# Optimization experiments

Hardware: AMD Instinct MI355X
Metric: run time of the kernel (lower is better)

## Reference

```python
import jax, jax.numpy as jnp
import numpy as np

B, N, H = 16, 128, 256


def setup_inputs() -> dict:
    key = jax.random.key(0)
    ks = jax.random.split(key, 7)
    s = 1.0 / np.sqrt(H)
    return {
        "inputs": jax.random.normal(ks[0], (B, N, H), dtype=jnp.float32),
        "bin_features": jax.random.normal(ks[1], (B, N, N, H), dtype=jnp.float32),
        "W_atom": jax.random.normal(ks[2], (H, H), dtype=jnp.float32) * s,
        "W_bin": jax.random.normal(ks[3], (H, H), dtype=jnp.float32) * s,
        "b_bin": jax.random.normal(ks[4], (H,), dtype=jnp.float32) * s,
        "w_score": jax.random.normal(ks[5], (H, 1), dtype=jnp.float32) * s,
        "b_score": jax.random.normal(ks[6], (1,), dtype=jnp.float32) * s,
    }


def reference(inputs, bin_features, W_atom, W_bin, b_bin, w_score, b_score):
    # atom_pair[b,i,j,h] = inputs[b,i,h] + inputs[b,j,h]
    atom_pair = inputs[:, :, None, :] + inputs[:, None, :, :]  # [B,N,N,H]
    # Linear(no bias) on atom_pair + Linear(bias) on bin_features, then ReLU.
    # Exploit linearity: (x_i + x_j) @ W = (x@W)_i + (x@W)_j to avoid an extra N^2 GEMM.
    xw = jnp.einsum('bnh,hk->bnk', inputs, W_atom)  # [B,N,H]
    att_hidden = jax.nn.relu(
        xw[:, :, None, :] + xw[:, None, :, :]
        + jnp.einsum('bijh,hk->bijk', bin_features, W_bin) + b_bin
    )  # [B,N,N,H]
    att_score = jnp.einsum('bijh,ho->bijo', att_hidden, w_score) + b_score  # [B,N,N,1]
    # att_context = att_score * inputs.unsqueeze(2); sum over j (dim 2)
    att_context = (att_score * inputs[:, :, None, :]).sum(axis=2)  # [B,N,H]
    return att_context, atom_pair
```

## Files before the change

kernel.cpp:

```cpp
#include <hip/hip_runtime.h>
#include <hip/hip_bf16.h>

#define H 256
#define NN 128
#define BB 16

typedef __attribute__((ext_vector_type(8))) __bf16 bf16x8;
typedef __attribute__((ext_vector_type(8))) short  s16x8;
typedef __attribute__((ext_vector_type(4))) short  s16x4;
typedef __attribute__((ext_vector_type(4))) float  f32x4;

__device__ __forceinline__ unsigned short f2b(float f) {
    unsigned u = __float_as_uint(f);
    u = (u + 0x7fffu + ((u >> 16) & 1u)) >> 16;
    return (unsigned short)u;
}

__global__ void k_prep_w(const float* __restrict__ Wb, unsigned short* __restrict__ WT) {
    int k = blockIdx.x;
    int h = threadIdx.x;
    WT[k * H + h] = f2b(Wb[h * H + k]);
}

__global__ void k_xw(const float* __restrict__ inp, const float* __restrict__ Wa,
                     float* __restrict__ xw) {
    __shared__ float rows[8][H];
    int r0 = blockIdx.x * 8;
    int t = threadIdx.x;
    #pragma unroll
    for (int r = 0; r < 8; ++r) rows[r][t] = inp[(r0 + r) * H + t];
    __syncthreads();
    float acc[8] = {0.f, 0.f, 0.f, 0.f, 0.f, 0.f, 0.f, 0.f};
    for (int h = 0; h < H; ++h) {
        float wv = Wa[h * H + t];
        #pragma unroll
        for (int r = 0; r < 8; ++r) acc[r] += rows[r][h] * wv;
    }
    #pragma unroll
    for (int r = 0; r < 8; ++r) xw[(r0 + r) * H + t] = acc[r];
}

__global__ __launch_bounds__(256) void k_main(
        const float* __restrict__ inp, const float* __restrict__ binf,
        const float* __restrict__ xw, const unsigned short* __restrict__ WT,
        const float* __restrict__ b_bin, const float* __restrict__ w_score,
        const float* __restrict__ b_score,
        float* __restrict__ out_ctx, float* __restrict__ out_pair) {
    __shared__ unsigned short Ab[64 * 260];
    __shared__ float base_l[H];
    __shared__ float wsc_l[H];
    __shared__ float ini_l[H];
    __shared__ float wred[4];
    __shared__ float Sp;

    int bid = blockIdx.x;
    int jt = bid & 1;
    int i  = (bid >> 1) & 127;
    int b  = bid >> 8;
    int t  = threadIdx.x;
    int bi = b * 128 + i;
    int jbase = jt * 64;

    base_l[t] = xw[bi * H + t] + b_bin[t];
    wsc_l[t]  = w_score[t];
    ini_l[t]  = inp[bi * H + t];

    const float4* bp = (const float4*)(binf + ((long)bi * 128 + jbase) * H);
    #pragma unroll
    for (int it = 0; it < 16; ++it) {
        int idx = it * 256 + t;
        float4 v = bp[idx];
        int row = idx >> 6;
        int col = (idx & 63) * 4;
        ushort4 w;
        w.x = f2b(v.x); w.y = f2b(v.y); w.z = f2b(v.z); w.w = f2b(v.w);
        *(ushort4*)&Ab[row * 260 + col] = w;
    }
    __syncthreads();

    int wave = t >> 6, lane = t & 63, q = lane >> 4, m16 = lane & 15;
    int colbase = wave * 64;

    f32x4 acc[4][4];
    #pragma unroll
    for (int rt = 0; rt < 4; ++rt)
        #pragma unroll
        for (int ct = 0; ct < 4; ++ct)
            acc[rt][ct] = (f32x4){0.f, 0.f, 0.f, 0.f};

    #pragma unroll
    for (int ks = 0; ks < 8; ++ks) {
        bf16x8 afr[4];
        #pragma unroll
        for (int rt = 0; rt < 4; ++rt) {
            const unsigned short* p = &Ab[(rt * 16 + m16) * 260 + ks * 32 + q * 8];
            s16x4 a0 = *(const s16x4*)p;
            s16x4 a1 = *(const s16x4*)(p + 4);
            s16x8 sv = __builtin_shufflevector(a0, a1, 0, 1, 2, 3, 4, 5, 6, 7);
            afr[rt] = __builtin_bit_cast(bf16x8, sv);
        }
        #pragma unroll
        for (int ct = 0; ct < 4; ++ct) {
            const unsigned short* wp = WT + (colbase + ct * 16 + m16) * H + ks * 32 + q * 8;
            bf16x8 bfr = __builtin_bit_cast(bf16x8, *(const s16x8*)wp);
            #pragma unroll
            for (int rt = 0; rt < 4; ++rt)
                acc[rt][ct] = __builtin_amdgcn_mfma_f32_16x16x32_bf16(afr[rt], bfr, acc[rt][ct], 0, 0, 0);
        }
    }

    float sacc = 0.f;
    const float* xwp = xw + ((long)b * 128 + jbase) * H;
    #pragma unroll
    for (int rt = 0; rt < 4; ++rt) {
        #pragma unroll
        for (int ct = 0; ct < 4; ++ct) {
            int k = colbase + ct * 16 + m16;
            float bs = base_l[k], wv = wsc_l[k];
            #pragma unroll
            for (int r = 0; r < 4; ++r) {
                int jl = rt * 16 + q * 4 + r;
                float hv = acc[rt][ct][r] + bs + xwp[jl * H + k];
                hv = fmaxf(hv, 0.f);
                sacc += hv * wv;
            }
        }
    }
    #pragma unroll
    for (int m = 1; m < 64; m <<= 1) sacc += __shfl_xor(sacc, m, 64);
    if (lane == 0) wred[wave] = sacc;
    __syncthreads();
    if (t == 0) Sp = wred[0] + wred[1] + wred[2] + wred[3] + 64.0f * b_score[0];
    __syncthreads();

    float iv = ini_l[t];
    float S  = Sp;
    const float* inb  = inp + ((long)b * 128 + jbase) * H;
    float* pout = out_pair + (((long)bi) * 128 + jbase) * H;
    #pragma unroll 4
    for (int j = 0; j < 64; ++j) {
        float v = inb[j * H + t];
        pout[j * H + t] = iv + v;
    }
    atomicAdd(&out_ctx[bi * H + t], iv * S);
}

extern "C" void kernel_launch(void* const* d_in, const int* in_sizes, int n_in,
                              void* d_out, int out_size, void* d_ws, size_t ws_size,
                              hipStream_t stream) {
    const float* inp     = (const float*)d_in[0];
    const float* binf    = (const float*)d_in[1];
    const float* W_atom  = (const float*)d_in[2];
    const float* W_bin   = (const float*)d_in[3];
    const float* b_bin   = (const float*)d_in[4];
    const float* w_score = (const float*)d_in[5];
    const float* b_score = (const float*)d_in[6];

    float* out_ctx  = (float*)d_out;
    float* out_pair = (float*)d_out + BB * NN * H;

    float* xw = (float*)d_ws;
    unsigned short* WT = (unsigned short*)((char*)d_ws + (size_t)BB * NN * H * 4);

    hipMemsetAsync(d_out, 0, (size_t)BB * NN * H * sizeof(float), stream);
    k_prep_w<<<H, H, 0, stream>>>(W_bin, WT);
    k_xw<<<BB * NN / 8, H, 0, stream>>>(inp, W_atom, xw);
    k_main<<<BB * NN * 2, 256, 0, stream>>>(inp, binf, xw, WT, b_bin, w_score,
                                            b_score, out_ctx, out_pair);
}
```

Before: 538.5 us.

## Split pair output into separate kernel and shrink score tiles to 32 rows

Moves the atom_pair broadcast-add into its own float4 streaming kernel and shrinks the score kernel's j-tile from 64 to 32 rows, so it launches four times as many blocks with half the LDS. The weight transpose now goes through a shared-memory tile for coalesced access, and the xw kernel uses 4 rows per block instead of 8. This aims to raise occupancy and separate the pure-bandwidth pair write from the GEMM path. In exchange it adds a launch and doubles the atomicAdd traffic to out_ctx, and the W_bin B-fragments are reused across fewer rows.

```diff
diff --git a/kernel.cpp b/kernel.cpp
--- a/kernel.cpp
+++ b/kernel.cpp
@@ -17,36 +17,68 @@
 }
 
 __global__ void k_prep_w(const float* __restrict__ Wb, unsigned short* __restrict__ WT) {
-    int k = blockIdx.x;
-    int h = threadIdx.x;
-    WT[k * H + h] = f2b(Wb[h * H + k]);
+    __shared__ float tile[32][33];
+    int tIdx = blockIdx.x;
+    int h0 = (tIdx >> 3) * 32, k0 = (tIdx & 7) * 32;
+    int tx = threadIdx.x & 31, ty = threadIdx.x >> 5;
+    #pragma unroll
+    for (int r = 0; r < 4; ++r) {
+        int h = ty + r * 8;
+        tile[h][tx] = Wb[(h0 + h) * H + k0 + tx];
+    }
+    __syncthreads();
+    #pragma unroll
+    for (int r = 0; r < 4; ++r) {
+        int k = ty + r * 8;
+        WT[(k0 + k) * H + h0 + tx] = f2b(tile[tx][k]);
+    }
 }
 
 __global__ void k_xw(const float* __restrict__ inp, const float* __restrict__ Wa,
                      float* __restrict__ xw) {
-    __shared__ float rows[8][H];
-    int r0 = blockIdx.x * 8;
+    __shared__ float rows[4][H];
+    int r0 = blockIdx.x * 4;
     int t = threadIdx.x;
     #pragma unroll
-    for (int r = 0; r < 8; ++r) rows[r][t] = inp[(r0 + r) * H + t];
+    for (int u = 0; u < 4; ++u) rows[u][t] = inp[(r0 + u) * H + t];
     __syncthreads();
-    float acc[8] = {0.f, 0.f, 0.f, 0.f, 0.f, 0.f, 0.f, 0.f};
+    float acc[4] = {0.f, 0.f, 0.f, 0.f};
+    #pragma unroll 8
     for (int h = 0; h < H; ++h) {
         float wv = Wa[h * H + t];
         #pragma unroll
-        for (int r = 0; r < 8; ++r) acc[r] += rows[r][h] * wv;
+        for (int u = 0; u < 4; ++u) acc[u] += rows[u][h] * wv;
     }
     #pragma unroll
-    for (int r = 0; r < 8; ++r) xw[(r0 + r) * H + t] = acc[r];
+    for (int u = 0; u < 4; ++u) xw[(r0 + u) * H + t] = acc[u];
 }
 
-__global__ __launch_bounds__(256) void k_main(
+__global__ __launch_bounds__(256) void k_pair(const float* __restrict__ inp,
+                                              float* __restrict__ out_pair) {
+    const float4* in4 = (const float4*)inp;
+    float4* o4 = (float4*)out_pair;
+    int tid = blockIdx.x * 256 + threadIdx.x;
+    #pragma unroll
+    for (int it = 0; it < 8; ++it) {
+        int idx = it * 2097152 + tid;
+        int h4 = idx & 63;
+        int j  = (idx >> 6) & 127;
+        int bi = idx >> 13;
+        int b  = bi >> 7;
+        float4 a = in4[bi * 64 + h4];
+        float4 c = in4[(b * 128 + j) * 64 + h4];
+        float4 r;
+        r.x = a.x + c.x; r.y = a.y + c.y; r.z = a.z + c.z; r.w = a.w + c.w;
+        o4[idx] = r;
+    }
+}
+
+__global__ __launch_bounds__(256) void k_score(
         const float* __restrict__ inp, const float* __restrict__ binf,
         const float* __restrict__ xw, const unsigned short* __restrict__ WT,
         const float* __restrict__ b_bin, const float* __restrict__ w_score,
-        const float* __restrict__ b_score,
-        float* __restrict__ out_ctx, float* __restrict__ out_pair) {
-    __shared__ unsigned short Ab[64 * 260];
+        const float* __restrict__ b_score, float* __restrict__ out_ctx) {
+    __shared__ unsigned short Ab[32 * 260];
     __shared__ float base_l[H];
     __shared__ float wsc_l[H];
     __shared__ float ini_l[H];
@@ -54,12 +86,12 @@
     __shared__ float Sp;
 
     int bid = blockIdx.x;
-    int jt = bid & 1;
-    int i  = (bid >> 1) & 127;
-    int b  = bid >> 8;
+    int jt = bid & 3;
+    int i  = (bid >> 2) & 127;
+    int b  = bid >> 9;
     int t  = threadIdx.x;
     int bi = b * 128 + i;
-    int jbase = jt * 64;
+    int jbase = jt * 32;
 
     base_l[t] = xw[bi * H + t] + b_bin[t];
     wsc_l[t]  = w_score[t];
@@ -67,7 +99,7 @@
 
     const float4* bp = (const float4*)(binf + ((long)bi * 128 + jbase) * H);
     #pragma unroll
-    for (int it = 0; it < 16; ++it) {
+    for (int it = 0; it < 8; ++it) {
         int idx = it * 256 + t;
         float4 v = bp[idx];
         int row = idx >> 6;
@@ -81,18 +113,18 @@
     int wave = t >> 6, lane = t & 63, q = lane >> 4, m16 = lane & 15;
     int colbase = wave * 64;
 
-    f32x4 acc[4][4];
+    f32x4 acc[2][4];
     #pragma unroll
-    for (int rt = 0; rt < 4; ++rt)
+    for (int rt = 0; rt < 2; ++rt)
         #pragma unroll
         for (int ct = 0; ct < 4; ++ct)
             acc[rt][ct] = (f32x4){0.f, 0.f, 0.f, 0.f};
 
     #pragma unroll
     for (int ks = 0; ks < 8; ++ks) {
-        bf16x8 afr[4];
+        bf16x8 afr[2];
         #pragma unroll
-        for (int rt = 0; rt < 4; ++rt) {
+        for (int rt = 0; rt < 2; ++rt) {
             const unsigned short* p = &Ab[(rt * 16 + m16) * 260 + ks * 32 + q * 8];
             s16x4 a0 = *(const s16x4*)p;
             s16x4 a1 = *(const s16x4*)(p + 4);
@@ -104,7 +136,7 @@
             const unsigned short* wp = WT + (colbase + ct * 16 + m16) * H + ks * 32 + q * 8;
             bf16x8 bfr = __builtin_bit_cast(bf16x8, *(const s16x8*)wp);
             #pragma unroll
-            for (int rt = 0; rt < 4; ++rt)
+            for (int rt = 0; rt < 2; ++rt)
                 acc[rt][ct] = __builtin_amdgcn_mfma_f32_16x16x32_bf16(afr[rt], bfr, acc[rt][ct], 0, 0, 0);
         }
     }
@@ -112,7 +144,7 @@
     float sacc = 0.f;
     const float* xwp = xw + ((long)b * 128 + jbase) * H;
     #pragma unroll
-    for (int rt = 0; rt < 4; ++rt) {
+    for (int rt = 0; rt < 2; ++rt) {
         #pragma unroll
         for (int ct = 0; ct < 4; ++ct) {
             int k = colbase + ct * 16 + m16;
@@ -130,19 +162,10 @@
     for (int m = 1; m < 64; m <<= 1) sacc += __shfl_xor(sacc, m, 64);
     if (lane == 0) wred[wave] = sacc;
     __syncthreads();
-    if (t == 0) Sp = wred[0] + wred[1] + wred[2] + wred[3] + 64.0f * b_score[0];
+    if (t == 0) Sp = wred[0] + wred[1] + wred[2] + wred[3] + 32.0f * b_score[0];
     __syncthreads();
 
-    float iv = ini_l[t];
-    float S  = Sp;
-    const float* inb  = inp + ((long)b * 128 + jbase) * H;
-    float* pout = out_pair + (((long)bi) * 128 + jbase) * H;
-    #pragma unroll 4
-    for (int j = 0; j < 64; ++j) {
-        float v = inb[j * H + t];
-        pout[j * H + t] = iv + v;
-    }
-    atomicAdd(&out_ctx[bi * H + t], iv * S);
+    atomicAdd(&out_ctx[bi * H + t], ini_l[t] * Sp);
 }
 
 extern "C" void kernel_launch(void* const* d_in, const int* in_sizes, int n_in,
@@ -163,8 +186,9 @@
     unsigned short* WT = (unsigned short*)((char*)d_ws + (size_t)BB * NN * H * 4);
 
     hipMemsetAsync(d_out, 0, (size_t)BB * NN * H * sizeof(float), stream);
-    k_prep_w<<<H, H, 0, stream>>>(W_bin, WT);
-    k_xw<<<BB * NN / 8, H, 0, stream>>>(inp, W_atom, xw);
-    k_main<<<BB * NN * 2, 256, 0, stream>>>(inp, binf, xw, WT, b_bin, w_score,
-                                            b_score, out_ctx, out_pair);
+    k_prep_w<<<64, 256, 0, stream>>>(W_bin, WT);
+    k_xw<<<BB * NN / 4, H, 0, stream>>>(inp, W_atom, xw);
+    k_pair<<<8192, 256, 0, stream>>>(inp, out_pair);
+    k_score<<<8192, 256, 0, stream>>>(inp, binf, xw, WT, b_bin, w_score,
+                                      b_score, out_ctx);
 }
```

Result: slower. 570.8 us (+6.0%).
